# Optimization experiments

Measured on AMD Instinct MI355X. Metric: run time of the kernel, lower is better.

Reference implementation:

```python
import jax, jax.numpy as jnp
import numpy as np

B, S, H, D = 4, 4096, 1024, 64

def setup_inputs() -> dict:
    key = jax.random.key(0)
    ks = jax.random.split(key, 10)
    return {
        "query": jax.random.normal(ks[0], (B, S, H), jnp.float32),
        "key": jax.random.normal(ks[1], (B, S, H), jnp.float32),
        "value": jax.random.normal(ks[2], (B, S, H), jnp.float32),
        "mask": jax.random.randint(ks[3], (B, S), 0, 2, jnp.int32),
        "Wq": jax.random.normal(ks[4], (H, D), jnp.float32) * 0.02,
        "bq": jax.random.normal(ks[5], (D,), jnp.float32) * 0.02,
        "Wk": jax.random.normal(ks[6], (H, D), jnp.float32) * 0.02,
        "bk": jax.random.normal(ks[7], (D,), jnp.float32) * 0.02,
        "Wv": jax.random.normal(ks[8], (H, D), jnp.float32) * 0.02,
        "bv": jax.random.normal(ks[9], (D,), jnp.float32) * 0.02,
    }

def reference(query, key, value, mask, Wq, bq, Wk, bk, Wv, bv):
    # single-head projections: [B,S,H] @ [H,D] -> [B,S,D]
    q = query @ Wq + bq
    k = key @ Wk + bk
    v = value @ Wv + bv
    scale = 1.0 / np.sqrt(D).astype(np.float32)
    # [B,Sq,Sk] score matrix (faithful to the unfused original)
    scores = jnp.einsum('bqd,bkd->bqk', q, k) * scale
    # mask [B,Sk] broadcast over query dim; masked positions -> -1e9
    scores = jnp.where(mask[:, None, :] == 0, jnp.float32(-1e9), scores)
    att = jax.nn.softmax(scores, axis=-1)
    # dropout prob = 0.0 -> identity
    return jnp.einsum('bqk,bkd->bqd', att, v)
```

## Files before the change

kernel.cpp:

```cpp
#include <hip/hip_runtime.h>
#include <hip/hip_bf16.h>
#include <stdint.h>


typedef __bf16 bf16;
typedef __bf16 bf16x8 __attribute__((ext_vector_type(8)));
typedef float f32x16 __attribute__((ext_vector_type(16)));

union B8 { uint4 u; bf16x8 v; uint32_t w[4]; };

#define AS1 __attribute__((address_space(1)))
#define AS3 __attribute__((address_space(3)))

__device__ __forceinline__ void async16(const void* g, void* l) {
  __builtin_amdgcn_global_load_lds((AS1 void*)(g), (AS3 void*)(l), 16, 0, 0);
}

#define KSC 0.18033688011112042f

__global__ void setup_kernel(const float* __restrict__ Wq, const float* __restrict__ Wk,
                             const float* __restrict__ Wv, const int* __restrict__ mask,
                             bf16* __restrict__ wT, float* __restrict__ biasArr)
{
  int item = blockIdx.x * 256 + threadIdx.x;
  if (item < 24576) {
    int mat = item >> 13;
    int rem = item & 8191;
    int n   = rem >> 7;
    int c   = rem & 127;
    const float* W = (mat == 0) ? Wq : (mat == 1) ? Wk : Wv;
    union { bf16 b[8]; uint4 u; } pk;
    #pragma unroll
    for (int j = 0; j < 8; ++j)
      pk.b[j] = (bf16)W[(c * 8 + j) * 64 + n];
    bf16* o = wT + mat * 65536;
    *(uint4*)(o + n * 1024 + c * 8) = pk.u;
  } else {
    int i = (item - 24576) << 2;
    const int4 m = *(const int4*)(mask + i);
    float4 b;
    b.x = m.x ? 0.0f : -1e30f;
    b.y = m.y ? 0.0f : -1e30f;
    b.z = m.z ? 0.0f : -1e30f;
    b.w = m.w ? 0.0f : -1e30f;
    *(float4*)(biasArr + i) = b;
  }
}

struct PF {
  float4 xa[4], xb[4];
  uint4  wa[4], wb[4];
};

__device__ __forceinline__ void load_chunk(const float* __restrict__ xr,
                                           const bf16* __restrict__ w0,
                                           const bf16* __restrict__ w1,
                                           int kc, PF& p) {
  #pragma unroll
  for (int s = 0; s < 4; ++s) {
    int k = kc + s * 16;
    p.xa[s] = *(const float4*)(xr + k);
    p.xb[s] = *(const float4*)(xr + k + 4);
    p.wa[s] = *(const uint4*)(w0 + k);
    p.wb[s] = *(const uint4*)(w1 + k);
  }
}

__device__ __forceinline__ void comp_chunk(const PF& p, f32x16& a0, f32x16& a1) {
  #pragma unroll
  for (int s = 0; s < 4; ++s) {
    union { bf16 b[8]; bf16x8 v; } af;
    af.b[0] = (bf16)p.xa[s].x; af.b[1] = (bf16)p.xa[s].y;
    af.b[2] = (bf16)p.xa[s].z; af.b[3] = (bf16)p.xa[s].w;
    af.b[4] = (bf16)p.xb[s].x; af.b[5] = (bf16)p.xb[s].y;
    af.b[6] = (bf16)p.xb[s].z; af.b[7] = (bf16)p.xb[s].w;
    B8 wa; wa.u = p.wa[s];
    B8 wb; wb.u = p.wb[s];
    a0 = __builtin_amdgcn_mfma_f32_32x32x16_bf16(af.v, wa.v, a0, 0, 0, 0);
    a1 = __builtin_amdgcn_mfma_f32_32x32x16_bf16(af.v, wb.v, a1, 0, 0, 0);
  }
}

__global__ __launch_bounds__(64, 2) void proj_kernel(
    const float* __restrict__ Xq, const float* __restrict__ Xk, const float* __restrict__ Xv,
    const bf16* __restrict__ wT,
    const float* __restrict__ bq, const float* __restrict__ bk, const float* __restrict__ bv,
    bf16* __restrict__ qo, bf16* __restrict__ ko, bf16* __restrict__ vTo)
{
  const int bx = blockIdx.x;
  const int mat = bx >> 9;
  const int m0 = (bx & 511) << 5;
  const float* X    = (mat == 0) ? Xq : (mat == 1) ? Xk : Xv;
  const float* bias = (mat == 0) ? bq : (mat == 1) ? bk : bv;
  const bf16* w = wT + mat * 65536;

  __shared__ __align__(16) bf16 cs[32 * 64];

  const int lane = threadIdx.x;
  const int half = lane >> 5;
  const int ln = lane & 31;

  const float* xr = X + (size_t)(m0 + ln) * 1024 + half * 8;
  const bf16*  w0 = w + ln * 1024 + half * 8;
  const bf16*  w1 = w + (ln + 32) * 1024 + half * 8;

  f32x16 acc0 = {};
  f32x16 acc1 = {};

  PF A, Bp;
  load_chunk(xr, w0, w1, 0, A);
  for (int c = 0; c < 16; c += 2) {
    load_chunk(xr, w0, w1, (c + 1) * 64, Bp);
    comp_chunk(A, acc0, acc1);
    if (c + 2 < 16) load_chunk(xr, w0, w1, (c + 2) * 64, A);
    comp_chunk(Bp, acc0, acc1);
  }

  {
    float b0v = bias[ln];
    float b1v = bias[ln + 32];
    #pragma unroll
    for (int r = 0; r < 16; ++r) {
      int mrow = (r & 3) + 8 * (r >> 2) + 4 * half;
      cs[mrow * 64 + ln]      = (bf16)(acc0[r] + b0v);
      cs[mrow * 64 + ln + 32] = (bf16)(acc1[r] + b1v);
    }
  }
  __syncthreads();

  if (mat < 2) {
    bf16* gout = (mat == 0) ? qo : ko;
    #pragma unroll
    for (int p = 0; p < 4; ++p) {
      int id = p * 64 + lane;
      int r = id >> 3;
      int c = id & 7;
      int phys = c ^ (r & 7);
      *(uint4*)(gout + (size_t)(m0 + r) * 64 + phys * 8) = *(const uint4*)(cs + r * 64 + c * 8);
    }
  } else {
    int batch = m0 >> 12;
    int sk = m0 & 4095;
    int tb = sk & ~63;
    int halfTile = (sk >> 5) & 1;
    #pragma unroll
    for (int p = 0; p < 4; ++p) {
      int id = p * 64 + lane;
      int d = id >> 2;
      int j = id & 3;
      union { bf16 b[8]; uint4 u; } pk;
      #pragma unroll
      for (int t = 0; t < 8; ++t) pk.b[t] = cs[(j * 8 + t) * 64 + d];
      int cl = halfTile * 4 + j;
      int phys = cl ^ (d & 7);
      *(uint4*)(vTo + ((size_t)batch * 64 + d) * 4096 + tb + phys * 8) = pk.u;
    }
  }
}

__global__ __launch_bounds__(256, 2) void flash_kernel(
    const bf16* __restrict__ qb, const bf16* __restrict__ kb, const bf16* __restrict__ vT,
    const float* __restrict__ biasArr, float* __restrict__ out)
{
  __shared__ __align__(16) char smem[65536];
  bf16* ksb = (bf16*)smem;
  bf16* vsb = (bf16*)(smem + 32768);

  const int tid = threadIdx.x;
  const int lane = tid & 63;
  const int wv = tid >> 6;
  const int half = lane >> 5;
  const int ln = lane & 31;

  const int batch = blockIdx.x >> 6;
  const int q0 = (blockIdx.x & 63) << 6;

  bf16x8 qf[2][4];
  const bf16* qbase = qb + ((size_t)batch * 4096 + q0) * 64;
  #pragma unroll
  for (int qk = 0; qk < 2; ++qk)
  #pragma unroll
  for (int s = 0; s < 4; ++s) {
    int qq = (qk << 5) + ln;
    int phys = (2 * s + half) ^ (qq & 7);
    B8 t; t.u = *(const uint4*)(qbase + qq * 64 + phys * 8);
    qf[qk][s] = t.v;
  }

  f32x16 acc[2][2] = {{{}, {}}, {{}, {}}};
  float den0 = 0.f, den1 = 0.f;

  bf16* kds = ksb + wv * 4096;
  bf16* vds = vsb + wv * 4096;
  const bf16* kgb = kb + (size_t)batch * 4096 * 64;
  const bf16* vgb = vT + (size_t)batch * 64 * 4096;
  const float* barr = biasArr + batch * 4096;

  for (int it = 0; it < 16; ++it) {
    const int key0 = wv * 1024 + it * 64;
    __syncthreads();
    const bf16* ksrc = kgb + (size_t)key0 * 64;
    #pragma unroll
    for (int i = 0; i < 8; ++i)
      async16((const char*)ksrc + i * 1024 + lane * 16, (char*)kds + i * 1024);
    const bf16* vsrc = vgb + key0;
    #pragma unroll
    for (int i = 0; i < 8; ++i)
      async16((const char*)vsrc + ((size_t)(i * 8 + (lane >> 3)) * 4096 + (lane & 7) * 8) * 2,
              (char*)vds + i * 1024);
    __syncthreads();

    #pragma unroll
    for (int st = 0; st < 2; ++st) {
      f32x16 s0 = {};
      f32x16 s1 = {};
      #pragma unroll
      for (int s = 0; s < 4; ++s) {
        int key = (st << 5) + ln;
        B8 af; af.u = *(const uint4*)(kds + key * 64 + (((2 * s + half) ^ (key & 7)) << 3));
        s0 = __builtin_amdgcn_mfma_f32_32x32x16_bf16(af.v, qf[0][s], s0, 0, 0, 0);
        s1 = __builtin_amdgcn_mfma_f32_32x32x16_bf16(af.v, qf[1][s], s1, 0, 0, 0);
      }
      float bb[16];
      #pragma unroll
      for (int g = 0; g < 4; ++g)
        *(float4*)&bb[4 * g] = *(const float4*)(barr + key0 + (st << 5) + 8 * g + (half << 2));
      uint32_t pk0[8], pk1[8];
      #pragma unroll
      for (int i = 0; i < 8; ++i) {
        float a0 = __builtin_amdgcn_exp2f(fmaf(s0[2 * i],     KSC, bb[2 * i]));
        float a1 = __builtin_amdgcn_exp2f(fmaf(s0[2 * i + 1], KSC, bb[2 * i + 1]));
        float c0 = __builtin_amdgcn_exp2f(fmaf(s1[2 * i],     KSC, bb[2 * i]));
        float c1 = __builtin_amdgcn_exp2f(fmaf(s1[2 * i + 1], KSC, bb[2 * i + 1]));
        den0 += a0 + a1;
        den1 += c0 + c1;
        union { bf16 b[2]; uint32_t u; } u0, u1;
        u0.b[0] = (bf16)a0; u0.b[1] = (bf16)a1;
        u1.b[0] = (bf16)c0; u1.b[1] = (bf16)c1;
        pk0[i] = u0.u; pk1[i] = u1.u;
      }
      uint32_t xp0[8], xp1[8];
      #pragma unroll
      for (int i = 0; i < 8; ++i) {
        xp0[i] = (uint32_t)__shfl_xor((int)pk0[i], 32);
        xp1[i] = (uint32_t)__shfl_xor((int)pk1[i], 32);
      }
      #pragma unroll
      for (int t = 0; t < 2; ++t) {
        B8 p0f, p1f;
        p0f.w[0] = half ? xp0[4 * t + 2] : pk0[4 * t];
        p0f.w[1] = half ? xp0[4 * t + 3] : pk0[4 * t + 1];
        p0f.w[2] = half ? pk0[4 * t + 2] : xp0[4 * t];
        p0f.w[3] = half ? pk0[4 * t + 3] : xp0[4 * t + 1];
        p1f.w[0] = half ? xp1[4 * t + 2] : pk1[4 * t];
        p1f.w[1] = half ? xp1[4 * t + 3] : pk1[4 * t + 1];
        p1f.w[2] = half ? pk1[4 * t + 2] : xp1[4 * t];
        p1f.w[3] = half ? pk1[4 * t + 3] : xp1[4 * t + 1];
        #pragma unroll
        for (int dh = 0; dh < 2; ++dh) {
          int d = (dh << 5) + ln;
          B8 vf; vf.u = *(const uint4*)(vds + d * 64 +
                          ((((st << 2) + (t << 1) + half) ^ (d & 7)) << 3));
          acc[0][dh] = __builtin_amdgcn_mfma_f32_32x32x16_bf16(vf.v, p0f.v, acc[0][dh], 0, 0, 0);
          acc[1][dh] = __builtin_amdgcn_mfma_f32_32x32x16_bf16(vf.v, p1f.v, acc[1][dh], 0, 0, 0);
        }
      }
    }
  }

  den0 += __shfl_xor(den0, 32);
  den1 += __shfl_xor(den1, 32);

  float* nb = (float*)smem;
  float* dn = (float*)(smem + 34816);

  __syncthreads();
  if (wv >= 2) {
    float* mynb = nb + (wv - 2) * 4352;
    #pragma unroll
    for (int qk = 0; qk < 2; ++qk)
    #pragma unroll
    for (int dh = 0; dh < 2; ++dh)
    #pragma unroll
    for (int g = 0; g < 4; ++g) {
      int q = (qk << 5) + ln;
      int d = 8 * g + (half << 2) + (dh << 5);
      f32x16 a = acc[qk][dh];
      *(float4*)(mynb + q * 68 + d) = make_float4(a[4*g], a[4*g+1], a[4*g+2], a[4*g+3]);
    }
    if (half == 0) {
      dn[(wv - 2) * 64 + ln]      = den0;
      dn[(wv - 2) * 64 + 32 + ln] = den1;
    }
  }
  __syncthreads();
  if (wv < 2) {
    float* pb = nb + wv * 4352;
    #pragma unroll
    for (int qk = 0; qk < 2; ++qk)
    #pragma unroll
    for (int dh = 0; dh < 2; ++dh)
    #pragma unroll
    for (int g = 0; g < 4; ++g) {
      int q = (qk << 5) + ln;
      int d = 8 * g + (half << 2) + (dh << 5);
      float4 t = *(const float4*)(pb + q * 68 + d);
      acc[qk][dh][4*g+0] += t.x; acc[qk][dh][4*g+1] += t.y;
      acc[qk][dh][4*g+2] += t.z; acc[qk][dh][4*g+3] += t.w;
    }
    den0 += dn[wv * 64 + ln];
    den1 += dn[wv * 64 + 32 + ln];
  }
  __syncthreads();
  if (wv < 2) {
    float* mynb = nb + wv * 4352;
    #pragma unroll
    for (int qk = 0; qk < 2; ++qk)
    #pragma unroll
    for (int dh = 0; dh < 2; ++dh)
    #pragma unroll
    for (int g = 0; g < 4; ++g) {
      int q = (qk << 5) + ln;
      int d = 8 * g + (half << 2) + (dh << 5);
      f32x16 a = acc[qk][dh];
      *(float4*)(mynb + q * 68 + d) = make_float4(a[4*g], a[4*g+1], a[4*g+2], a[4*g+3]);
    }
    if (half == 0) {
      dn[wv * 64 + ln]      = den0;
      dn[wv * 64 + 32 + ln] = den1;
    }
  }
  __syncthreads();
  #pragma unroll
  for (int p = 0; p < 4; ++p) {
    int i = p * 256 + tid;
    int qq = i >> 4;
    int d4 = (i & 15) << 2;
    float4 A = *(const float4*)(nb + qq * 68 + d4);
    float4 Bv = *(const float4*)(nb + 4352 + qq * 68 + d4);
    float dd = dn[qq] + dn[64 + qq];
    float inv = 1.0f / dd;
    float4 o = make_float4((A.x + Bv.x) * inv, (A.y + Bv.y) * inv,
                           (A.z + Bv.z) * inv, (A.w + Bv.w) * inv);
    *(float4*)(out + ((size_t)batch * 4096 + q0 + qq) * 64 + d4) = o;
  }
}

extern "C" void kernel_launch(void* const* d_in, const int* in_sizes, int n_in,
                              void* d_out, int out_size, void* d_ws, size_t ws_size,
                              hipStream_t stream)
{
  const float* query = (const float*)d_in[0];
  const float* key   = (const float*)d_in[1];
  const float* value = (const float*)d_in[2];
  const int*   mask  = (const int*)d_in[3];
  const float* Wq    = (const float*)d_in[4];
  const float* bq    = (const float*)d_in[5];
  const float* Wk    = (const float*)d_in[6];
  const float* bk    = (const float*)d_in[7];
  const float* Wv    = (const float*)d_in[8];
  const float* bv    = (const float*)d_in[9];
  float* out = (float*)d_out;

  bf16* qb = (bf16*)d_ws;
  bf16* kb = qb + 1048576;
  bf16* vT = kb + 1048576;
  bf16* wT = vT + 1048576;
  float* biasArr = (float*)((char*)d_ws + 3 * 2097152 + 393216);

  setup_kernel<<<112, 256, 0, stream>>>(Wq, Wk, Wv, mask, wT, biasArr);
  proj_kernel<<<1536, 64, 0, stream>>>(query, key, value, wT, bq, bk, bv, qb, kb, vT);
  flash_kernel<<<256, 256, 0, stream>>>(qb, kb, vT, biasArr, out);
}
```

Baseline: 283.8 us.

## Stage projection activations through LDS with async double-buffered global loads

The projection kernel now streams each 32x64 fp32 activation chunk into a double-buffered, XOR-swizzled LDS tile using global_load_lds, rather than each lane loading strided rows straight into registers. Weights are still prefetched into registers one chunk ahead, and manual vmcnt waits sequence the loads. The aim is coalesced 16-byte activation loads and fewer live registers. In exchange it uses 16KB more LDS per block, drops the min-blocks launch bound, and relies on hand-written waitcnt counts being correct for a single-wave block without barriers.

```diff
diff --git a/kernel.cpp b/kernel.cpp
--- a/kernel.cpp
+++ b/kernel.cpp
@@ -47,41 +47,7 @@
   }
 }
 
-struct PF {
-  float4 xa[4], xb[4];
-  uint4  wa[4], wb[4];
-};
-
-__device__ __forceinline__ void load_chunk(const float* __restrict__ xr,
-                                           const bf16* __restrict__ w0,
-                                           const bf16* __restrict__ w1,
-                                           int kc, PF& p) {
-  #pragma unroll
-  for (int s = 0; s < 4; ++s) {
-    int k = kc + s * 16;
-    p.xa[s] = *(const float4*)(xr + k);
-    p.xb[s] = *(const float4*)(xr + k + 4);
-    p.wa[s] = *(const uint4*)(w0 + k);
-    p.wb[s] = *(const uint4*)(w1 + k);
-  }
-}
-
-__device__ __forceinline__ void comp_chunk(const PF& p, f32x16& a0, f32x16& a1) {
-  #pragma unroll
-  for (int s = 0; s < 4; ++s) {
-    union { bf16 b[8]; bf16x8 v; } af;
-    af.b[0] = (bf16)p.xa[s].x; af.b[1] = (bf16)p.xa[s].y;
-    af.b[2] = (bf16)p.xa[s].z; af.b[3] = (bf16)p.xa[s].w;
-    af.b[4] = (bf16)p.xb[s].x; af.b[5] = (bf16)p.xb[s].y;
-    af.b[6] = (bf16)p.xb[s].z; af.b[7] = (bf16)p.xb[s].w;
-    B8 wa; wa.u = p.wa[s];
-    B8 wb; wb.u = p.wb[s];
-    a0 = __builtin_amdgcn_mfma_f32_32x32x16_bf16(af.v, wa.v, a0, 0, 0, 0);
-    a1 = __builtin_amdgcn_mfma_f32_32x32x16_bf16(af.v, wb.v, a1, 0, 0, 0);
-  }
-}
-
-__global__ __launch_bounds__(64, 2) void proj_kernel(
+__global__ __launch_bounds__(64) void proj_kernel(
     const float* __restrict__ Xq, const float* __restrict__ Xk, const float* __restrict__ Xv,
     const bf16* __restrict__ wT,
     const float* __restrict__ bq, const float* __restrict__ bk, const float* __restrict__ bv,
@@ -94,37 +60,85 @@
   const float* bias = (mat == 0) ? bq : (mat == 1) ? bk : bv;
   const bf16* w = wT + mat * 65536;
 
+  __shared__ __align__(16) float xbuf[2][32 * 64];
   __shared__ __align__(16) bf16 cs[32 * 64];
 
   const int lane = threadIdx.x;
   const int half = lane >> 5;
   const int ln = lane & 31;
 
-  const float* xr = X + (size_t)(m0 + ln) * 1024 + half * 8;
+  const int drow = lane >> 4;
+  const int dcl  = lane & 15;
+
+  const float* xb = X + (size_t)m0 * 1024;
   const bf16*  w0 = w + ln * 1024 + half * 8;
   const bf16*  w1 = w + (ln + 32) * 1024 + half * 8;
 
+  float b0v = bias[ln];
+  float b1v = bias[ln + 32];
+  asm volatile("s_waitcnt vmcnt(0)" ::: "memory");
+
+  #pragma unroll
+  for (int i = 0; i < 8; ++i) {
+    int row = i * 4 + drow;
+    int sc = (dcl & 8) | ((dcl ^ (row & 7)) & 7);
+    async16(xb + (size_t)row * 1024 + sc * 4, &xbuf[0][i * 256]);
+  }
+  uint4 wc0[4], wc1[4], wn0[4], wn1[4];
+  #pragma unroll
+  for (int s = 0; s < 4; ++s) {
+    wc0[s] = *(const uint4*)(w0 + s * 16);
+    wc1[s] = *(const uint4*)(w1 + s * 16);
+  }
+
   f32x16 acc0 = {};
   f32x16 acc1 = {};
 
-  PF A, Bp;
-  load_chunk(xr, w0, w1, 0, A);
-  for (int c = 0; c < 16; c += 2) {
-    load_chunk(xr, w0, w1, (c + 1) * 64, Bp);
-    comp_chunk(A, acc0, acc1);
-    if (c + 2 < 16) load_chunk(xr, w0, w1, (c + 2) * 64, A);
-    comp_chunk(Bp, acc0, acc1);
-  }
-
-  {
-    float b0v = bias[ln];
-    float b1v = bias[ln + 32];
-    #pragma unroll
-    for (int r = 0; r < 16; ++r) {
-      int mrow = (r & 3) + 8 * (r >> 2) + 4 * half;
-      cs[mrow * 64 + ln]      = (bf16)(acc0[r] + b0v);
-      cs[mrow * 64 + ln + 32] = (bf16)(acc1[r] + b1v);
-    }
+  for (int c = 0; c < 16; ++c) {
+    if (c < 15) {
+      const float* src = xb + (c + 1) * 64;
+      #pragma unroll
+      for (int i = 0; i < 8; ++i) {
+        int row = i * 4 + drow;
+        int sc = (dcl & 8) | ((dcl ^ (row & 7)) & 7);
+        async16(src + (size_t)row * 1024 + sc * 4, &xbuf[(c + 1) & 1][i * 256]);
+      }
+      #pragma unroll
+      for (int s = 0; s < 4; ++s) {
+        wn0[s] = *(const uint4*)(w0 + (c + 1) * 64 + s * 16);
+        wn1[s] = *(const uint4*)(w1 + (c + 1) * 64 + s * 16);
+      }
+      asm volatile("s_waitcnt vmcnt(16)" ::: "memory");
+    } else {
+      asm volatile("s_waitcnt vmcnt(0)" ::: "memory");
+    }
+    const float* xl = &xbuf[c & 1][0];
+    #pragma unroll
+    for (int s = 0; s < 4; ++s) {
+      int lc = s * 4 + half * 2;
+      int p0 = (lc & 8) | ((lc ^ (ln & 7)) & 7);
+      int p1 = ((lc + 1) & 8) | (((lc + 1) ^ (ln & 7)) & 7);
+      float4 fa = *(const float4*)(xl + ln * 64 + p0 * 4);
+      float4 fb = *(const float4*)(xl + ln * 64 + p1 * 4);
+      union { bf16 b[8]; bf16x8 v; } af;
+      af.b[0] = (bf16)fa.x; af.b[1] = (bf16)fa.y;
+      af.b[2] = (bf16)fa.z; af.b[3] = (bf16)fa.w;
+      af.b[4] = (bf16)fb.x; af.b[5] = (bf16)fb.y;
+      af.b[6] = (bf16)fb.z; af.b[7] = (bf16)fb.w;
+      B8 wa; wa.u = wc0[s];
+      B8 wb; wb.u = wc1[s];
+      acc0 = __builtin_amdgcn_mfma_f32_32x32x16_bf16(af.v, wa.v, acc0, 0, 0, 0);
+      acc1 = __builtin_amdgcn_mfma_f32_32x32x16_bf16(af.v, wb.v, acc1, 0, 0, 0);
+    }
+    #pragma unroll
+    for (int s = 0; s < 4; ++s) { wc0[s] = wn0[s]; wc1[s] = wn1[s]; }
+  }
+
+  #pragma unroll
+  for (int r = 0; r < 16; ++r) {
+    int mrow = (r & 3) + 8 * (r >> 2) + 4 * half;
+    cs[mrow * 64 + ln]      = (bf16)(acc0[r] + b0v);
+    cs[mrow * 64 + ln + 32] = (bf16)(acc1[r] + b1v);
   }
   __syncthreads();
 
```

Result: faster. 264.2 us (-6.9%).
